# Performance work log

Measured on AMD Instinct MI355X. Metric: run time of the kernel, lower is better.

## Reference

```python
import jax, jax.numpy as jnp
import numpy as np

B, IN, E, NCLS = 1024, 784, 256, 10
BRAIN, ADIM, NJUMPS = 4, 3, 4
N = BRAIN ** ADIM  # 64 blocks
TAU = 1.0
_GKEY = jax.random.key(42)  # fixed key -> deterministic gumbel noise


def _gumbel_softmax_hard(key, logits):
    u = jax.random.uniform(key, logits.shape, minval=1e-6, maxval=1.0 - 1e-6)
    g = -jnp.log(-jnp.log(u))
    y = jax.nn.softmax((logits + g) / TAU, axis=-1)
    hard = jax.nn.one_hot(jnp.argmax(y, axis=-1), logits.shape[-1], dtype=y.dtype)
    return jax.lax.stop_gradient(hard - y) + y  # straight-through


def _next_address(state, key, at0_W1, at0_b1, at0_W2, at0_b2):
    # always uses block 0's address_transform (as in the original forward)
    h = jax.nn.relu(state @ at0_W1 + at0_b1)
    logits = (h @ at0_W2 + at0_b2).reshape(state.shape[0], ADIM, BRAIN)
    return _gumbel_softmax_hard(key, logits)  # (B, ADIM, BRAIN) one-hot


def _all_blocks(state, st_W1, st_b1, st_W2, st_b2):
    # state: (B,E); st_W*: (N,E,E) stored (in,out). Two batched GEMMs over all N blocks.
    h = jax.nn.relu(jnp.einsum('be,neh->bnh', state, st_W1) + st_b1[None])
    h = jax.nn.relu(jnp.einsum('bnh,nhg->bng', h, st_W2) + st_b2[None])
    norm = jnp.linalg.norm(state, axis=1, keepdims=True)  # (B,1), norm of INPUT state
    return h / (norm[:, :, None] + 1e-6)  # (B,N,E)


def _flatten_onehot(oh):
    # (B, ADIM, BRAIN) -> (B, BRAIN**ADIM) via iterated outer product
    b = oh.shape[0]
    fw = oh[:, 0, :]
    for d in range(1, oh.shape[1]):
        fw = (fw[:, :, None] * oh[:, d, None, :]).reshape(b, -1)
    return fw


def _forward(x, W_emb, b_emb, st_W1, st_b1, st_W2, st_b2,
             at0_W1, at0_b1, at0_W2, at0_b2, out_W1, out_b1, out_W2, out_b2):
    bsz = x.shape[0]
    state = x.reshape(bsz, -1) @ W_emb + b_emb
    initial_state = state
    current_address = _next_address(state, jax.random.fold_in(_GKEY, 0),
                                    at0_W1, at0_b1, at0_W2, at0_b2)
    exited = jnp.zeros((bsz,), dtype=bool)
    exit_states = jnp.zeros_like(state)
    exit_addresses = jnp.zeros_like(current_address)
    for i in range(NJUMPS):  # fixed small jump count; early-break replaced by masking (same math)
        active = ~exited
        bw = _flatten_onehot(current_address)                      # (B,N)
        allout = _all_blocks(state, st_W1, st_b1, st_W2, st_b2)    # (B,N,E)
        new_state = jnp.einsum('bn,bne->be', bw, allout)
        new_address = _next_address(new_state, jax.random.fold_in(_GKEY, i + 1),
                                    at0_W1, at0_b1, at0_W2, at0_b2)
        idx = jnp.argmax(new_address, axis=2)
        is_origin = jnp.all(idx == 0, axis=1) & active
        exit_states = jnp.where(is_origin[:, None], new_state, exit_states)
        exit_addresses = jnp.where(is_origin[:, None, None], new_address, exit_addresses)
        exited = exited | is_origin
        state = jnp.where(active[:, None], new_state, state)
        current_address = jnp.where(active[:, None, None], new_address, current_address)
    final_address = jnp.where(exited[:, None, None], exit_addresses, current_address)
    bw = _flatten_onehot(final_address)
    # original code computes block_out twice and keeps the one using `state` (bug-faithful)
    allout = _all_blocks(state, st_W1, st_b1, st_W2, st_b2)
    final_output = jnp.einsum('bn,bne->be', bw, allout) + initial_state
    h = jax.nn.relu(final_output @ out_W1 + out_b1)
    return h @ out_W2 + out_b2  # (B, NCLS)


def setup_inputs() -> dict:
    key = jax.random.key(0)
    ks = jax.random.split(key, 16)
    s = 0.02
    return {
        'x': jax.random.normal(ks[0], (B, IN), jnp.float32),
        'W_emb': jax.random.normal(ks[1], (IN, E), jnp.float32) * s,
        'b_emb': jnp.zeros((E,), jnp.float32),
        'st_W1': jax.random.normal(ks[2], (N, E, E), jnp.float32) * s,
        'st_b1': jnp.zeros((N, E), jnp.float32),
        'st_W2': jax.random.normal(ks[3], (N, E, E), jnp.float32) * s,
        'st_b2': jnp.zeros((N, E), jnp.float32),
        'at0_W1': jax.random.normal(ks[4], (E, E), jnp.float32) * s,
        'at0_b1': jnp.zeros((E,), jnp.float32),
        'at0_W2': jax.random.normal(ks[5], (E, ADIM * BRAIN), jnp.float32) * s,
        'at0_b2': jnp.zeros((ADIM * BRAIN,), jnp.float32),
        'out_W1': jax.random.normal(ks[6], (E, E), jnp.float32) * s,
        'out_b1': jnp.zeros((E,), jnp.float32),
        'out_W2': jax.random.normal(ks[7], (E, NCLS), jnp.float32) * s,
        'out_b2': jnp.zeros((NCLS,), jnp.float32),
    }


def reference(x, W_emb, b_emb, st_W1, st_b1, st_W2, st_b2,
              at0_W1, at0_b1, at0_W2, at0_b2, out_W1, out_b1, out_W2, out_b2):
    return _forward(x, W_emb, b_emb, st_W1, st_b1, st_W2, st_b2,
                    at0_W1, at0_b1, at0_W2, at0_b2, out_W1, out_b1, out_W2, out_b2)
```

## Files before the change

### kernel.cpp

```cpp
#include <hip/hip_runtime.h>
#include <stdint.h>


#define BATCH 1024
#define EDIM  256
#define INDIM 784
#define CH    4
#define GRID_B 304

__host__ __device__ inline uint32_t rotl32(uint32_t x, uint32_t d) {
  return (x << d) | (x >> (32u - d));
}
__host__ __device__ inline void threefry2x32(uint32_t k0, uint32_t k1,
                                             uint32_t x0, uint32_t x1,
                                             uint32_t* o0, uint32_t* o1) {
  uint32_t ks2 = k0 ^ k1 ^ 0x1BD11BDAu;
  x0 += k0; x1 += k1;
#define TF_R(a) { x0 += x1; x1 = rotl32(x1, a); x1 ^= x0; }
  TF_R(13) TF_R(15) TF_R(26) TF_R(6)   x0 += k1;  x1 += ks2 + 1u;
  TF_R(17) TF_R(29) TF_R(16) TF_R(24)  x0 += ks2; x1 += k0  + 2u;
  TF_R(13) TF_R(15) TF_R(26) TF_R(6)   x0 += k0;  x1 += k1  + 3u;
  TF_R(17) TF_R(29) TF_R(16) TF_R(24)  x0 += k1;  x1 += ks2 + 4u;
  TF_R(13) TF_R(15) TF_R(26) TF_R(6)   x0 += ks2; x1 += k0  + 5u;
#undef TF_R
  *o0 = x0; *o1 = x1;
}
__device__ inline uint32_t jax_bits12288(uint32_t k0, uint32_t k1, uint32_t L) {
  uint32_t o0, o1;
  if (L < 6144u) { threefry2x32(k0, k1, L, L + 6144u, &o0, &o1); return o0; }
  else           { threefry2x32(k0, k1, L - 6144u, L, &o0, &o1); return o1; }
}
__device__ inline float jax_uniform(uint32_t bits) {
  const float minv = 1e-6f;
  const float maxv = (float)(1.0 - 1e-06);
  const float span = maxv - minv;
  uint32_t fb = (bits >> 9) | 0x3f800000u;
  float f = __uint_as_float(fb) - 1.0f;
  float u = __fadd_rn(__fmul_rn(f, span), minv);
  return fmaxf(minv, u);
}
__device__ inline float gumbel_val(int s, int b, int c) {
  uint32_t fk0, fk1;
  threefry2x32(0u, 42u, 0u, (uint32_t)s, &fk0, &fk1);
  const uint32_t L = (uint32_t)(b * 12 + c);
  const float u = jax_uniform(jax_bits12288(fk0, fk1, L));
  return -logf(-logf(u));
}
__device__ inline int addr_argmax(const float* v) {
  int i0 = 0, i1 = 0, i2 = 0;
  { float b = v[0];
    for (int c = 1; c < 4; c++) { float x = v[c];     if (x > b) { b = x; i0 = c; } } }
  { float b = v[4];
    for (int c = 1; c < 4; c++) { float x = v[4 + c]; if (x > b) { b = x; i1 = c; } } }
  { float b = v[8];
    for (int c = 1; c < 4; c++) { float x = v[8 + c]; if (x > b) { b = x; i2 = c; } } }
  return i0 * 16 + i1 * 4 + i2;
}

#define LDW16(dst, Wc, kkq)                                                     \
  { _Pragma("unroll")                                                           \
    for (int _q = 0; _q < 4; _q++) {                                            \
      _Pragma("unroll")                                                         \
      for (int _cc = 0; _cc < 4; _cc++)                                         \
        dst[_q * 4 + _cc] = (Wc)[(size_t)((kkq) + _q) * EDIM + _cc * 64];       \
    } }

#define FMA16(acc, wv, XSarr, SROW, kabs)                                       \
  { const float4 _r0 = *(const float4*)&(XSarr)[0 * (SROW) + (kabs)];           \
    const float4 _r1 = *(const float4*)&(XSarr)[1 * (SROW) + (kabs)];           \
    const float4 _r2 = *(const float4*)&(XSarr)[2 * (SROW) + (kabs)];           \
    const float4 _r3 = *(const float4*)&(XSarr)[3 * (SROW) + (kabs)];           \
    _Pragma("unroll")                                                           \
    for (int _cc = 0; _cc < 4; _cc++) {                                         \
      acc[0][_cc] = fmaf(_r0.x, wv[0 + _cc], acc[0][_cc]);                      \
      acc[0][_cc] = fmaf(_r0.y, wv[4 + _cc], acc[0][_cc]);                      \
      acc[0][_cc] = fmaf(_r0.z, wv[8 + _cc], acc[0][_cc]);                      \
      acc[0][_cc] = fmaf(_r0.w, wv[12 + _cc], acc[0][_cc]);                     \
      acc[1][_cc] = fmaf(_r1.x, wv[0 + _cc], acc[1][_cc]);                      \
      acc[1][_cc] = fmaf(_r1.y, wv[4 + _cc], acc[1][_cc]);                      \
      acc[1][_cc] = fmaf(_r1.z, wv[8 + _cc], acc[1][_cc]);                      \
      acc[1][_cc] = fmaf(_r1.w, wv[12 + _cc], acc[1][_cc]);                     \
      acc[2][_cc] = fmaf(_r2.x, wv[0 + _cc], acc[2][_cc]);                      \
      acc[2][_cc] = fmaf(_r2.y, wv[4 + _cc], acc[2][_cc]);                      \
      acc[2][_cc] = fmaf(_r2.z, wv[8 + _cc], acc[2][_cc]);                      \
      acc[2][_cc] = fmaf(_r2.w, wv[12 + _cc], acc[2][_cc]);                     \
      acc[3][_cc] = fmaf(_r3.x, wv[0 + _cc], acc[3][_cc]);                      \
      acc[3][_cc] = fmaf(_r3.y, wv[4 + _cc], acc[3][_cc]);                      \
      acc[3][_cc] = fmaf(_r3.z, wv[8 + _cc], acc[3][_cc]);                      \
      acc[3][_cc] = fmaf(_r3.w, wv[12 + _cc], acc[3][_cc]);                     \
    } }

#define GEMM_TILE(Wbase, XSarr, SROW, kb, KS, acc)                              \
  { const float* _Wc = (Wbase) + (size_t)(kb) * EDIM + jc;                      \
    float _wvA[16], _wvB[16];                                                   \
    LDW16(_wvA, _Wc, 0)                                                         \
    _Pragma("unroll 1")                                                         \
    for (int _kk = 0; _kk < (KS); _kk += 8) {                                   \
      LDW16(_wvB, _Wc, _kk + 4)                                                 \
      FMA16(acc, _wvA, XSarr, SROW, (kb) + _kk)                                 \
      if (_kk + 8 < (KS)) LDW16(_wvA, _Wc, _kk + 8)                             \
      FMA16(acc, _wvB, XSarr, SROW, (kb) + _kk + 4)                             \
    } }

#define FMA16H(acc, wv, Harr, kabs)                                             \
  { _Pragma("unroll")                                                           \
    for (int _q = 0; _q < 4; _q++) {                                            \
      const float4 _h = *(const float4*)&(Harr)[((kabs) + _q) * 4];             \
      _Pragma("unroll")                                                         \
      for (int _cc = 0; _cc < 4; _cc++) {                                       \
        acc[0][_cc] = fmaf(_h.x, wv[_q * 4 + _cc], acc[0][_cc]);                \
        acc[1][_cc] = fmaf(_h.y, wv[_q * 4 + _cc], acc[1][_cc]);                \
        acc[2][_cc] = fmaf(_h.z, wv[_q * 4 + _cc], acc[2][_cc]);                \
        acc[3][_cc] = fmaf(_h.w, wv[_q * 4 + _cc], acc[3][_cc]);                \
      } } }

#define GEMM_TILE_H(Wbase, Harr, kb, KS, acc)                                   \
  { const float* _Wc = (Wbase) + (size_t)(kb) * EDIM + jc;                      \
    float _wvA[16], _wvB[16];                                                   \
    LDW16(_wvA, _Wc, 0)                                                         \
    _Pragma("unroll 1")                                                         \
    for (int _kk = 0; _kk < (KS); _kk += 8) {                                   \
      LDW16(_wvB, _Wc, _kk + 4)                                                 \
      FMA16H(acc, _wvA, Harr, (kb) + _kk)                                       \
      if (_kk + 8 < (KS)) LDW16(_wvA, _Wc, _kk + 8)                             \
      FMA16H(acc, _wvB, Harr, (kb) + _kk + 4)                                   \
    } }

#define P_STORE(P, kg, jc, acc)                                                 \
  { _Pragma("unroll")                                                           \
    for (int _cc = 0; _cc < 4; _cc++) {                                         \
      const int _col = (jc) + _cc * 64;                                         \
      *(float4*)&(P)[(((kg) * 256) + _col) * 4] =                               \
        make_float4(acc[0][_cc], acc[1][_cc], acc[2][_cc], acc[3][_cc]);        \
    } }

#define P_REDUCE8(P, col, bias, dst4)                                           \
  { float4 _ps = *(const float4*)&(P)[(col) * 4];                               \
    _Pragma("unroll")                                                           \
    for (int _pw = 1; _pw < 8; _pw++) {                                         \
      const float4 _pp = *(const float4*)&(P)[((_pw * 256) + (col)) * 4];       \
      _ps.x += _pp.x; _ps.y += _pp.y; _ps.z += _pp.z; _ps.w += _pp.w;           \
    }                                                                           \
    _ps.x += (bias); _ps.y += (bias); _ps.z += (bias); _ps.w += (bias);         \
    dst4 = _ps; }

#define ADDR_TAIL(P, H, P2a, vals, ab1, aW2, ab2, astep, ROWEXPR)               \
  { if (t < 256) {                                                              \
      float4 s; P_REDUCE8(P, t, (ab1)[t], s);                                   \
      *(float4*)&(H)[t * 4] = make_float4(fmaxf(s.x, 0.f), fmaxf(s.y, 0.f),     \
                                          fmaxf(s.z, 0.f), fmaxf(s.w, 0.f));    \
    }                                                                           \
    __syncthreads();                                                            \
    { const int c = t & 15, ksl = t >> 4;                                       \
      float a2[4] = {0.f, 0.f, 0.f, 0.f};                                       \
      if (c < 12) {                                                             \
        const int k0 = ksl * 8;                                                 \
        _Pragma("unroll")                                                       \
        for (int k = k0; k < k0 + 8; k++) {                                     \
          const float4 h = *(const float4*)&(H)[k * 4];                         \
          const float w = (aW2)[k * 12 + c];                                    \
          a2[0] = fmaf(h.x, w, a2[0]); a2[1] = fmaf(h.y, w, a2[1]);             \
          a2[2] = fmaf(h.z, w, a2[2]); a2[3] = fmaf(h.w, w, a2[3]);             \
        }                                                                       \
      }                                                                         \
      *(float4*)&(P2a)[(ksl * 16 + c) * 4] = make_float4(a2[0], a2[1], a2[2], a2[3]); \
    }                                                                           \
    __syncthreads();                                                            \
    if (t < 48) {                                                               \
      const int i = t / 12, c = t % 12;                                         \
      float s = 0.f;                                                            \
      _Pragma("unroll")                                                         \
      for (int w = 0; w < 32; w++) s += (P2a)[(w * 16 + c) * 4 + i];            \
      (vals)[i * 12 + c] = s + (ab2)[c] + gumbel_val((astep), (ROWEXPR), c);    \
    }                                                                           \
    __syncthreads();                                                            \
  }

__global__ __launch_bounds__(512, 2) void k_embed_a0(
    const float* __restrict__ x, const float* __restrict__ Wemb,
    const float* __restrict__ bemb,
    const float* __restrict__ aW1, const float* __restrict__ ab1,
    const float* __restrict__ aW2, const float* __restrict__ ab2,
    float* __restrict__ state, float* __restrict__ initial,
    int* __restrict__ nn_all) {
  __shared__ __align__(16) float XS[4 * INDIM];
  __shared__ __align__(16) float P[8 * 256 * 4];
  __shared__ __align__(16) float SS[4 * EDIM];
  __shared__ __align__(16) float H[EDIM * 4];
  __shared__ __align__(16) float P2a[32 * 16 * 4];
  __shared__ float vals[4 * 12];
  const int t = threadIdx.x, b0 = blockIdx.x * 4;
  const int jc = t & 63, kg = t >> 6;

  { const float4* src = (const float4*)(x + (size_t)b0 * INDIM);
    for (int p = t; p < INDIM; p += 512) ((float4*)XS)[p] = src[p];
  }
  __syncthreads();

  {
    const int kb = (kg < 2) ? kg * 104 : 208 + (kg - 2) * 96;
    float acc[4][4] = {};
    if (kg < 2) { GEMM_TILE(Wemb, XS, INDIM, kb, 104, acc); }
    else        { GEMM_TILE(Wemb, XS, INDIM, kb, 96, acc); }
    P_STORE(P, kg, jc, acc);
  }
  __syncthreads();
  if (t < 256) {
    float4 s; P_REDUCE8(P, t, bemb[t], s);
    SS[0 * EDIM + t] = s.x; SS[1 * EDIM + t] = s.y;
    SS[2 * EDIM + t] = s.z; SS[3 * EDIM + t] = s.w;
    state[(size_t)(b0 + 0) * EDIM + t] = s.x; initial[(size_t)(b0 + 0) * EDIM + t] = s.x;
    state[(size_t)(b0 + 1) * EDIM + t] = s.y; initial[(size_t)(b0 + 1) * EDIM + t] = s.y;
    state[(size_t)(b0 + 2) * EDIM + t] = s.z; initial[(size_t)(b0 + 2) * EDIM + t] = s.z;
    state[(size_t)(b0 + 3) * EDIM + t] = s.w; initial[(size_t)(b0 + 3) * EDIM + t] = s.w;
  }
  __syncthreads();

  {
    const int kb = kg * 32;
    float acc[4][4] = {};
    GEMM_TILE(aW1, SS, EDIM, kb, 32, acc);
    P_STORE(P, kg, jc, acc);
  }
  __syncthreads();
  ADDR_TAIL(P, H, P2a, vals, ab1, aW2, ab2, 0, b0 + i);
  if (t < 4) nn_all[b0 + t] = addr_argmax(&vals[t * 12]);
}

#define B_ROUTE(nnval_expr)                                                     \
  if (t < 64) hist[t] = 0;                                                      \
  if (t < 4) rowsl[t] = 0;                                                      \
  __syncthreads();                                                              \
  int myv[2]; bool fl[2];                                                       \
  _Pragma("unroll")                                                             \
  for (int p = 0; p < 2; p++) {                                                 \
    const int rr = p * 512 + t;                                                 \
    myv[p] = (nnval_expr);                                                      \
    if (myv[p] >= 0) atomicAdd(&hist[myv[p]], 1);                               \
  }                                                                             \
  __syncthreads();                                                              \
  if (t < 64) {                                                                 \
    const int cnt = hist[t];                                                    \
    const int nch = (cnt + CH - 1) / CH;                                        \
    int icnt = cnt, inch = nch;                                                 \
    _Pragma("unroll")                                                           \
    for (int d = 1; d < 64; d <<= 1) {                                          \
      int t1 = __shfl_up(icnt, d), t2 = __shfl_up(inch, d);                     \
      if (t >= d) { icnt += t1; inch += t2; }                                   \
    }                                                                           \
    const int ench = inch - nch;                                                \
    if (t == 63) meta[3] = inch;                                                \
    if (c >= ench && c < ench + nch) {                                          \
      meta[0] = t; meta[1] = c - ench;                                          \
      meta[2] = min(CH, cnt - (c - ench) * CH);                                 \
    }                                                                           \
  }                                                                             \
  __syncthreads();                                                              \
  if (c >= meta[3]) return;                                                     \
  const int n = meta[0], local = meta[1], m = meta[2];                          \
  {                                                                             \
    const int wid = t >> 6, lane = t & 63;                                      \
    unsigned long long bals[2];                                                 \
    _Pragma("unroll")                                                           \
    for (int p = 0; p < 2; p++) {                                               \
      fl[p] = (myv[p] == n);                                                    \
      bals[p] = __ballot(fl[p]);                                                \
      if (lane == 0) wcnt2[p * 8 + wid] = __popcll(bals[p]);                    \
    }                                                                           \
    __syncthreads();                                                            \
    if (t == 0) { int s = 0;                                                    \
      for (int e = 0; e < 16; e++) { wbase2[e] = s; s += wcnt2[e]; } }          \
    __syncthreads();                                                            \
    const int r0 = local * CH;                                                  \
    _Pragma("unroll")                                                           \
    for (int p = 0; p < 2; p++) {                                               \
      if (fl[p]) {                                                              \
        const int rank = wbase2[p * 8 + wid] +                                  \
          __popcll(bals[p] & ((1ull << lane) - 1ull));                          \
        if (rank >= r0 && rank < r0 + CH) rowsl[rank - r0] = p * 512 + t;       \
      }                                                                         \
    }                                                                           \
    __syncthreads();                                                            \
  }

__global__ __launch_bounds__(512, 2) void k_block_mid(
    float* __restrict__ state,
    const float* __restrict__ W1, const float* __restrict__ b1,
    const float* __restrict__ W2, const float* __restrict__ b2,
    const float* __restrict__ aW1, const float* __restrict__ ab1,
    const float* __restrict__ aW2, const float* __restrict__ ab2,
    int* __restrict__ nn_all, int rstep) {
  __shared__ __align__(16) float XS[4 * EDIM];
  __shared__ __align__(16) float P[8 * 256 * 4];
  __shared__ __align__(16) float H[EDIM * 4];
  __shared__ __align__(16) float P2a[32 * 16 * 4];
  __shared__ float vals[4 * 12];
  __shared__ int hist[64], meta[4], rowsl[4];
  __shared__ int wcnt2[16], wbase2[16];
  __shared__ float denom[4];
  const int t = threadIdx.x;
  const int c = ((blockIdx.x & 7) * 38) + (blockIdx.x >> 3);
  const int jc = t & 63, kg = t >> 6;
  const int* nnj = nn_all + rstep * BATCH;

  B_ROUTE(nnj[rr])

  if (t < 256) {
    const int i = t >> 6, q = t & 63;
    const int row = rowsl[min(i, m - 1)] & 1023;
    const float4 v = *(const float4*)(state + (size_t)row * EDIM + q * 4);
    ((float4*)XS)[t] = v;
    float sq = v.x * v.x + v.y * v.y + v.z * v.z + v.w * v.w;
#pragma unroll
    for (int d = 32; d >= 1; d >>= 1) sq += __shfl_xor(sq, d);
    if (q == 0) denom[i] = sqrtf(sq) + 1e-6f;
  }
  __syncthreads();

  const float* W1n = W1 + (size_t)n * EDIM * EDIM;
  const float* W2n = W2 + (size_t)n * EDIM * EDIM;
  const int kb = kg * 32;
  { float acc[4][4] = {};
    GEMM_TILE(W1n, XS, EDIM, kb, 32, acc);
    P_STORE(P, kg, jc, acc);
  }
  __syncthreads();
  if (t < 256) {
    float4 s; P_REDUCE8(P, t, b1[(size_t)n * EDIM + t], s);
    *(float4*)&H[t * 4] = make_float4(fmaxf(s.x, 0.f), fmaxf(s.y, 0.f),
                                      fmaxf(s.z, 0.f), fmaxf(s.w, 0.f));
  }
  __syncthreads();
  { float acc[4][4] = {};
    GEMM_TILE_H(W2n, H, kb, 32, acc);
    P_STORE(P, kg, jc, acc);
  }
  __syncthreads();
  if (t < 256) {
    float4 s; P_REDUCE8(P, t, b2[(size_t)n * EDIM + t], s);
    float sv[4] = { s.x, s.y, s.z, s.w };
#pragma unroll
    for (int i = 0; i < 4; i++) {
      if (i < m) {
        const int row = rowsl[i] & 1023;
        const float v = fmaxf(sv[i], 0.f) / denom[i];
        state[(size_t)row * EDIM + t] = v;
        XS[i * EDIM + t] = v;
      }
    }
  }
  __syncthreads();

  { float acc[4][4] = {};
    GEMM_TILE(aW1, XS, EDIM, kb, 32, acc);
    P_STORE(P, kg, jc, acc);
  }
  __syncthreads();
  ADDR_TAIL(P, H, P2a, vals, ab1, aW2, ab2, rstep + 1, (rowsl[i] & 1023));
  if (t < m) {
    const int b = rowsl[t] & 1023;
    const int nn = addr_argmax(&vals[t * 12]);
    const int s = rstep + 1;
    if (s < 4) {
      if (nn == 0) {
        for (int q = s; q <= 4; q++) nn_all[q * BATCH + b] = -1;
      } else nn_all[s * BATCH + b] = nn;
    } else nn_all[4 * BATCH + b] = nn;
  }
}

__global__ __launch_bounds__(512, 2) void k_block_final(
    const float* __restrict__ state,
    const float* __restrict__ W1, const float* __restrict__ b1,
    const float* __restrict__ W2, const float* __restrict__ b2,
    const float* __restrict__ initial,
    const float* __restrict__ oW1, const float* __restrict__ ob1,
    const float* __restrict__ oW2, const float* __restrict__ ob2,
    const int* __restrict__ nn4, float* __restrict__ out) {
  __shared__ __align__(16) float XS[4 * EDIM];
  __shared__ __align__(16) float P[8 * 256 * 4];
  __shared__ __align__(16) float H[EDIM * 4];
  __shared__ __align__(16) float P2h[32 * 16 * 4];
  __shared__ int hist[64], meta[4], rowsl[4];
  __shared__ int wcnt2[16], wbase2[16];
  __shared__ float denom[4];
  const int t = threadIdx.x;
  const int c = ((blockIdx.x & 7) * 38) + (blockIdx.x >> 3);
  const int jc = t & 63, kg = t >> 6;

  B_ROUTE(max(nn4[rr], 0))

  if (t < 256) {
    const int i = t >> 6, q = t & 63;
    const int row = rowsl[min(i, m - 1)] & 1023;
    const float4 v = *(const float4*)(state + (size_t)row * EDIM + q * 4);
    ((float4*)XS)[t] = v;
    float sq = v.x * v.x + v.y * v.y + v.z * v.z + v.w * v.w;
#pragma unroll
    for (int d = 32; d >= 1; d >>= 1) sq += __shfl_xor(sq, d);
    if (q == 0) denom[i] = sqrtf(sq) + 1e-6f;
  }
  __syncthreads();

  const float* W1n = W1 + (size_t)n * EDIM * EDIM;
  const float* W2n = W2 + (size_t)n * EDIM * EDIM;
  const int kb = kg * 32;
  { float acc[4][4] = {};
    GEMM_TILE(W1n, XS, EDIM, kb, 32, acc);
    P_STORE(P, kg, jc, acc);
  }
  __syncthreads();
  if (t < 256) {
    float4 s; P_REDUCE8(P, t, b1[(size_t)n * EDIM + t], s);
    *(float4*)&H[t * 4] = make_float4(fmaxf(s.x, 0.f), fmaxf(s.y, 0.f),
                                      fmaxf(s.z, 0.f), fmaxf(s.w, 0.f));
  }
  __syncthreads();
  { float acc[4][4] = {};
    GEMM_TILE_H(W2n, H, kb, 32, acc);
    P_STORE(P, kg, jc, acc);
  }
  __syncthreads();
  if (t < 256) {
    float4 s; P_REDUCE8(P, t, b2[(size_t)n * EDIM + t], s);
    float sv[4] = { s.x, s.y, s.z, s.w };
#pragma unroll
    for (int i = 0; i < 4; i++) {
      const int row = rowsl[i] & 1023;
      float v = fmaxf(sv[i], 0.f) / denom[i];
      v += initial[(size_t)row * EDIM + t];
      XS[i * EDIM + t] = v;
    }
  }
  __syncthreads();

  { float acc[4][4] = {};
    GEMM_TILE(oW1, XS, EDIM, kb, 32, acc);
    P_STORE(P, kg, jc, acc);
  }
  __syncthreads();
  if (t < 256) {
    float4 s; P_REDUCE8(P, t, ob1[t], s);
    *(float4*)&H[t * 4] = make_float4(fmaxf(s.x, 0.f), fmaxf(s.y, 0.f),
                                      fmaxf(s.z, 0.f), fmaxf(s.w, 0.f));
  }
  __syncthreads();
  {
    const int cc = t & 15, ksl = t >> 4;
    float a2[4] = {0.f, 0.f, 0.f, 0.f};
    if (cc < 10) {
      const int k0 = ksl * 8;
#pragma unroll
      for (int k = k0; k < k0 + 8; k++) {
        const float4 h = *(const float4*)&H[k * 4];
        const float w = oW2[k * 10 + cc];
        a2[0] = fmaf(h.x, w, a2[0]); a2[1] = fmaf(h.y, w, a2[1]);
        a2[2] = fmaf(h.z, w, a2[2]); a2[3] = fmaf(h.w, w, a2[3]);
      }
    }
    *(float4*)&P2h[(ksl * 16 + cc) * 4] = make_float4(a2[0], a2[1], a2[2], a2[3]);
  }
  __syncthreads();
  if (t < 40) {
    const int i = t / 10, cc = t % 10;
    if (i < m) {
      float s = 0.f;
#pragma unroll
      for (int w = 0; w < 32; w++) s += P2h[(w * 16 + cc) * 4 + i];
      const int row = rowsl[i] & 1023;
      out[(size_t)row * 10 + cc] = s + ob2[cc];
    }
  }
}

extern "C" void kernel_launch(void* const* d_in, const int* in_sizes, int n_in,
                              void* d_out, int out_size, void* d_ws, size_t ws_size,
                              hipStream_t stream) {
  const float* x    = (const float*)d_in[0];
  const float* Wemb = (const float*)d_in[1];
  const float* bemb = (const float*)d_in[2];
  const float* stW1 = (const float*)d_in[3];
  const float* stb1 = (const float*)d_in[4];
  const float* stW2 = (const float*)d_in[5];
  const float* stb2 = (const float*)d_in[6];
  const float* aW1  = (const float*)d_in[7];
  const float* ab1  = (const float*)d_in[8];
  const float* aW2  = (const float*)d_in[9];
  const float* ab2  = (const float*)d_in[10];
  const float* oW1  = (const float*)d_in[11];
  const float* ob1  = (const float*)d_in[12];
  const float* oW2  = (const float*)d_in[13];
  const float* ob2  = (const float*)d_in[14];
  float* out = (float*)d_out;

  char* ws = (char*)d_ws;
  auto alloc = [&](size_t bytes) { char* p = ws; ws += (bytes + 255) & ~(size_t)255; return p; };
  float* state   = (float*)alloc((size_t)BATCH * EDIM * 4);
  float* initial = (float*)alloc((size_t)BATCH * EDIM * 4);
  int*   nn_all  = (int*)alloc(5 * BATCH * 4);

  k_embed_a0<<<BATCH / 4, 512, 0, stream>>>(x, Wemb, bemb, aW1, ab1, aW2, ab2,
                                            state, initial, nn_all);
  for (int j = 0; j < 4; j++)
    k_block_mid<<<GRID_B, 512, 0, stream>>>(state, stW1, stb1, stW2, stb2,
                                            aW1, ab1, aW2, ab2, nn_all, j);
  k_block_final<<<GRID_B, 512, 0, stream>>>(state, stW1, stb1, stW2, stb2,
                                            initial, oW1, ob1, oW2, ob2,
                                            nn_all + 4 * BATCH, out);
}
```

Measured before the change: 231.3 us.

## Process eight rows per block in routed block GEMMs and split embed/address kernels

Doubles the number of batch rows handled per workgroup in the routed block-MLP kernels (CH 4→8, fewer blocks), reshaping each thread's tile to 8 rows × 2 columns with 4 k-partitions instead of 8. Each weight element loaded from global memory is reused across more rows, so per-expert weight traffic falls. The fused embed+address kernel is also split into a column-split embed kernel and a separate address kernel. The cost is fewer workgroups (less parallelism, with more rounding waste when an expert gets a partial group of rows), more register pressure, and one extra kernel launch.

New measurement: 243.1 us. 1.05x slower.

```diff
diff --git a/kernel.cpp b/kernel.cpp
--- a/kernel.cpp
+++ b/kernel.cpp
@@ -5,8 +5,8 @@
 #define BATCH 1024
 #define EDIM  256
 #define INDIM 784
-#define CH    4
-#define GRID_B 304
+#define CH    8
+#define GRID_B 192
 
 __host__ __device__ inline uint32_t rotl32(uint32_t x, uint32_t d) {
   return (x << d) | (x >> (32u - d));
@@ -57,179 +57,207 @@
   return i0 * 16 + i1 * 4 + i2;
 }
 
-#define LDW16(dst, Wc, kkq)                                                     \
+#define LDW8(dst, Wc, kkq, CSTR)                                                \
   { _Pragma("unroll")                                                           \
     for (int _q = 0; _q < 4; _q++) {                                            \
       _Pragma("unroll")                                                         \
-      for (int _cc = 0; _cc < 4; _cc++)                                         \
-        dst[_q * 4 + _cc] = (Wc)[(size_t)((kkq) + _q) * EDIM + _cc * 64];       \
+      for (int _cc = 0; _cc < 2; _cc++)                                         \
+        dst[_q * 2 + _cc] = (Wc)[(size_t)((kkq) + _q) * EDIM + _cc * (CSTR)];   \
     } }
 
-#define FMA16(acc, wv, XSarr, SROW, kabs)                                       \
+#define FMA_ROW(acc, ri, rv, wv)                                                \
+  acc[ri][0] = fmaf(rv.x, wv[0], acc[ri][0]);                                   \
+  acc[ri][0] = fmaf(rv.y, wv[2], acc[ri][0]);                                   \
+  acc[ri][0] = fmaf(rv.z, wv[4], acc[ri][0]);                                   \
+  acc[ri][0] = fmaf(rv.w, wv[6], acc[ri][0]);                                   \
+  acc[ri][1] = fmaf(rv.x, wv[1], acc[ri][1]);                                   \
+  acc[ri][1] = fmaf(rv.y, wv[3], acc[ri][1]);                                   \
+  acc[ri][1] = fmaf(rv.z, wv[5], acc[ri][1]);                                   \
+  acc[ri][1] = fmaf(rv.w, wv[7], acc[ri][1]);
+
+#define FMA32(acc, wv, XSarr, SROW, kabs)                                       \
   { const float4 _r0 = *(const float4*)&(XSarr)[0 * (SROW) + (kabs)];           \
     const float4 _r1 = *(const float4*)&(XSarr)[1 * (SROW) + (kabs)];           \
     const float4 _r2 = *(const float4*)&(XSarr)[2 * (SROW) + (kabs)];           \
     const float4 _r3 = *(const float4*)&(XSarr)[3 * (SROW) + (kabs)];           \
-    _Pragma("unroll")                                                           \
-    for (int _cc = 0; _cc < 4; _cc++) {                                         \
-      acc[0][_cc] = fmaf(_r0.x, wv[0 + _cc], acc[0][_cc]);                      \
-      acc[0][_cc] = fmaf(_r0.y, wv[4 + _cc], acc[0][_cc]);                      \
-      acc[0][_cc] = fmaf(_r0.z, wv[8 + _cc], acc[0][_cc]);                      \
-      acc[0][_cc] = fmaf(_r0.w, wv[12 + _cc], acc[0][_cc]);                     \
-      acc[1][_cc] = fmaf(_r1.x, wv[0 + _cc], acc[1][_cc]);                      \
-      acc[1][_cc] = fmaf(_r1.y, wv[4 + _cc], acc[1][_cc]);                      \
-      acc[1][_cc] = fmaf(_r1.z, wv[8 + _cc], acc[1][_cc]);                      \
-      acc[1][_cc] = fmaf(_r1.w, wv[12 + _cc], acc[1][_cc]);                     \
-      acc[2][_cc] = fmaf(_r2.x, wv[0 + _cc], acc[2][_cc]);                      \
-      acc[2][_cc] = fmaf(_r2.y, wv[4 + _cc], acc[2][_cc]);                      \
-      acc[2][_cc] = fmaf(_r2.z, wv[8 + _cc], acc[2][_cc]);                      \
-      acc[2][_cc] = fmaf(_r2.w, wv[12 + _cc], acc[2][_cc]);                     \
-      acc[3][_cc] = fmaf(_r3.x, wv[0 + _cc], acc[3][_cc]);                      \
-      acc[3][_cc] = fmaf(_r3.y, wv[4 + _cc], acc[3][_cc]);                      \
-      acc[3][_cc] = fmaf(_r3.z, wv[8 + _cc], acc[3][_cc]);                      \
-      acc[3][_cc] = fmaf(_r3.w, wv[12 + _cc], acc[3][_cc]);                     \
-    } }
-
-#define GEMM_TILE(Wbase, XSarr, SROW, kb, KS, acc)                              \
-  { const float* _Wc = (Wbase) + (size_t)(kb) * EDIM + jc;                      \
-    float _wvA[16], _wvB[16];                                                   \
-    LDW16(_wvA, _Wc, 0)                                                         \
+    const float4 _r4 = *(const float4*)&(XSarr)[4 * (SROW) + (kabs)];           \
+    const float4 _r5 = *(const float4*)&(XSarr)[5 * (SROW) + (kabs)];           \
+    const float4 _r6 = *(const float4*)&(XSarr)[6 * (SROW) + (kabs)];           \
+    const float4 _r7 = *(const float4*)&(XSarr)[7 * (SROW) + (kabs)];           \
+    FMA_ROW(acc, 0, _r0, wv) FMA_ROW(acc, 1, _r1, wv)                           \
+    FMA_ROW(acc, 2, _r2, wv) FMA_ROW(acc, 3, _r3, wv)                           \
+    FMA_ROW(acc, 4, _r4, wv) FMA_ROW(acc, 5, _r5, wv)                           \
+    FMA_ROW(acc, 6, _r6, wv) FMA_ROW(acc, 7, _r7, wv) }
+
+#define GEMM_TILE8(Wbase, COLB, CSTR, XSarr, SROW, kb, KS, acc)                 \
+  { const float* _Wc = (Wbase) + (size_t)(kb) * EDIM + (COLB);                  \
+    float _wvA[8], _wvB[8];                                                     \
+    LDW8(_wvA, _Wc, 0, CSTR)                                                    \
     _Pragma("unroll 1")                                                         \
     for (int _kk = 0; _kk < (KS); _kk += 8) {                                   \
-      LDW16(_wvB, _Wc, _kk + 4)                                                 \
-      FMA16(acc, _wvA, XSarr, SROW, (kb) + _kk)                                 \
-      if (_kk + 8 < (KS)) LDW16(_wvA, _Wc, _kk + 8)                             \
-      FMA16(acc, _wvB, XSarr, SROW, (kb) + _kk + 4)                             \
+      LDW8(_wvB, _Wc, _kk + 4, CSTR)                                            \
+      FMA32(acc, _wvA, XSarr, SROW, (kb) + _kk)                                 \
+      if (_kk + 8 < (KS)) LDW8(_wvA, _Wc, _kk + 8, CSTR)                        \
+      FMA32(acc, _wvB, XSarr, SROW, (kb) + _kk + 4)                             \
     } }
 
-#define FMA16H(acc, wv, Harr, kabs)                                             \
+#define FMA32H(acc, wv, Harr, kabs)                                             \
   { _Pragma("unroll")                                                           \
     for (int _q = 0; _q < 4; _q++) {                                            \
-      const float4 _h = *(const float4*)&(Harr)[((kabs) + _q) * 4];             \
+      const float4 _hl = *(const float4*)&(Harr)[((kabs) + _q) * 8];            \
+      const float4 _hh = *(const float4*)&(Harr)[((kabs) + _q) * 8 + 4];        \
       _Pragma("unroll")                                                         \
-      for (int _cc = 0; _cc < 4; _cc++) {                                       \
-        acc[0][_cc] = fmaf(_h.x, wv[_q * 4 + _cc], acc[0][_cc]);                \
-        acc[1][_cc] = fmaf(_h.y, wv[_q * 4 + _cc], acc[1][_cc]);                \
-        acc[2][_cc] = fmaf(_h.z, wv[_q * 4 + _cc], acc[2][_cc]);                \
-        acc[3][_cc] = fmaf(_h.w, wv[_q * 4 + _cc], acc[3][_cc]);                \
+      for (int _cc = 0; _cc < 2; _cc++) {                                       \
+        acc[0][_cc] = fmaf(_hl.x, wv[_q * 2 + _cc], acc[0][_cc]);               \
+        acc[1][_cc] = fmaf(_hl.y, wv[_q * 2 + _cc], acc[1][_cc]);               \
+        acc[2][_cc] = fmaf(_hl.z, wv[_q * 2 + _cc], acc[2][_cc]);               \
+        acc[3][_cc] = fmaf(_hl.w, wv[_q * 2 + _cc], acc[3][_cc]);               \
+        acc[4][_cc] = fmaf(_hh.x, wv[_q * 2 + _cc], acc[4][_cc]);               \
+        acc[5][_cc] = fmaf(_hh.y, wv[_q * 2 + _cc], acc[5][_cc]);               \
+        acc[6][_cc] = fmaf(_hh.z, wv[_q * 2 + _cc], acc[6][_cc]);               \
+        acc[7][_cc] = fmaf(_hh.w, wv[_q * 2 + _cc], acc[7][_cc]);               \
       } } }
 
-#define GEMM_TILE_H(Wbase, Harr, kb, KS, acc)                                   \
-  { const float* _Wc = (Wbase) + (size_t)(kb) * EDIM + jc;                      \
-    float _wvA[16], _wvB[16];                                                   \
-    LDW16(_wvA, _Wc, 0)                                                         \
+#define GEMM_TILE_H8(Wbase, COLB, CSTR, Harr, kb, KS, acc)                      \
+  { const float* _Wc = (Wbase) + (size_t)(kb) * EDIM + (COLB);                  \
+    float _wvA[8], _wvB[8];                                                     \
+    LDW8(_wvA, _Wc, 0, CSTR)                                                    \
     _Pragma("unroll 1")                                                         \
     for (int _kk = 0; _kk < (KS); _kk += 8) {                                   \
-      LDW16(_wvB, _Wc, _kk + 4)                                                 \
-      FMA16H(acc, _wvA, Harr, (kb) + _kk)                                       \
-      if (_kk + 8 < (KS)) LDW16(_wvA, _Wc, _kk + 8)                             \
-      FMA16H(acc, _wvB, Harr, (kb) + _kk + 4)                                   \
+      LDW8(_wvB, _Wc, _kk + 4, CSTR)                                            \
+      FMA32H(acc, _wvA, Harr, (kb) + _kk)                                       \
+      if (_kk + 8 < (KS)) LDW8(_wvA, _Wc, _kk + 8, CSTR)                        \
+      FMA32H(acc, _wvB, Harr, (kb) + _kk + 4)                                   \
     } }
 
-#define P_STORE(P, kg, jc, acc)                                                 \
+#define P_STORE8(P, kg, NCOL, LCOL, CSTR, acc)                                  \
   { _Pragma("unroll")                                                           \
-    for (int _cc = 0; _cc < 4; _cc++) {                                         \
-      const int _col = (jc) + _cc * 64;                                         \
-      *(float4*)&(P)[(((kg) * 256) + _col) * 4] =                               \
+    for (int _cc = 0; _cc < 2; _cc++) {                                         \
+      const int _col = (LCOL) + _cc * (CSTR);                                   \
+      *(float4*)&(P)[(((kg) * (NCOL)) + _col) * 8] =                            \
         make_float4(acc[0][_cc], acc[1][_cc], acc[2][_cc], acc[3][_cc]);        \
+      *(float4*)&(P)[(((kg) * (NCOL)) + _col) * 8 + 4] =                        \
+        make_float4(acc[4][_cc], acc[5][_cc], acc[6][_cc], acc[7][_cc]);        \
     } }
 
-#define P_REDUCE8(P, col, bias, dst4)                                           \
-  { float4 _ps = *(const float4*)&(P)[(col) * 4];                               \
+#define P_REDUCE(P, col, NCOL, NPART, bias, lo4, hi4)                           \
+  { lo4 = *(const float4*)&(P)[(col) * 8];                                      \
+    hi4 = *(const float4*)&(P)[(col) * 8 + 4];                                  \
     _Pragma("unroll")                                                           \
-    for (int _pw = 1; _pw < 8; _pw++) {                                         \
-      const float4 _pp = *(const float4*)&(P)[((_pw * 256) + (col)) * 4];       \
-      _ps.x += _pp.x; _ps.y += _pp.y; _ps.z += _pp.z; _ps.w += _pp.w;           \
-    }                                                                           \
-    _ps.x += (bias); _ps.y += (bias); _ps.z += (bias); _ps.w += (bias);         \
-    dst4 = _ps; }
-
-#define ADDR_TAIL(P, H, P2a, vals, ab1, aW2, ab2, astep, ROWEXPR)               \
+    for (int _pw = 1; _pw < (NPART); _pw++) {                                   \
+      const float4 _pl = *(const float4*)&(P)[((_pw * (NCOL)) + (col)) * 8];    \
+      const float4 _ph = *(const float4*)&(P)[((_pw * (NCOL)) + (col)) * 8 + 4];\
+      lo4.x += _pl.x; lo4.y += _pl.y; lo4.z += _pl.z; lo4.w += _pl.w;           \
+      hi4.x += _ph.x; hi4.y += _ph.y; hi4.z += _ph.z; hi4.w += _ph.w;           \
+    }                                                                           \
+    lo4.x += (bias); lo4.y += (bias); lo4.z += (bias); lo4.w += (bias);         \
+    hi4.x += (bias); hi4.y += (bias); hi4.z += (bias); hi4.w += (bias); }
+
+#define ADDR_TAIL8(P, H, P2a, vals, ab1, aW2, ab2, astep, ROWEXPR)              \
   { if (t < 256) {                                                              \
-      float4 s; P_REDUCE8(P, t, (ab1)[t], s);                                   \
-      *(float4*)&(H)[t * 4] = make_float4(fmaxf(s.x, 0.f), fmaxf(s.y, 0.f),     \
-                                          fmaxf(s.z, 0.f), fmaxf(s.w, 0.f));    \
+      float4 lo, hi; P_REDUCE(P, t, 256, 4, (ab1)[t], lo, hi);                  \
+      *(float4*)&(H)[t * 8] = make_float4(fmaxf(lo.x, 0.f), fmaxf(lo.y, 0.f),   \
+                                          fmaxf(lo.z, 0.f), fmaxf(lo.w, 0.f));  \
+      *(float4*)&(H)[t * 8 + 4] = make_float4(fmaxf(hi.x, 0.f), fmaxf(hi.y, 0.f),\
+                                              fmaxf(hi.z, 0.f), fmaxf(hi.w, 0.f));\
     }                                                                           \
     __syncthreads();                                                            \
     { const int c = t & 15, ksl = t >> 4;                                       \
-      float a2[4] = {0.f, 0.f, 0.f, 0.f};                                       \
+      float a2[8] = {0.f,0.f,0.f,0.f,0.f,0.f,0.f,0.f};                          \
       if (c < 12) {                                                             \
         const int k0 = ksl * 8;                                                 \
         _Pragma("unroll")                                                       \
         for (int k = k0; k < k0 + 8; k++) {                                     \
-          const float4 h = *(const float4*)&(H)[k * 4];                         \
+          const float4 hl = *(const float4*)&(H)[k * 8];                        \
+          const float4 hh = *(const float4*)&(H)[k * 8 + 4];                    \
           const float w = (aW2)[k * 12 + c];                                    \
-          a2[0] = fmaf(h.x, w, a2[0]); a2[1] = fmaf(h.y, w, a2[1]);             \
-          a2[2] = fmaf(h.z, w, a2[2]); a2[3] = fmaf(h.w, w, a2[3]);             \
+          a2[0] = fmaf(hl.x, w, a2[0]); a2[1] = fmaf(hl.y, w, a2[1]);           \
+          a2[2] = fmaf(hl.z, w, a2[2]); a2[3] = fmaf(hl.w, w, a2[3]);           \
+          a2[4] = fmaf(hh.x, w, a2[4]); a2[5] = fmaf(hh.y, w, a2[5]);           \
+          a2[6] = fmaf(hh.z, w, a2[6]); a2[7] = fmaf(hh.w, w, a2[7]);           \
         }                                                                       \
       }                                                                         \
-      *(float4*)&(P2a)[(ksl * 16 + c) * 4] = make_float4(a2[0], a2[1], a2[2], a2[3]); \
+      *(float4*)&(P2a)[(ksl * 16 + c) * 8] = make_float4(a2[0], a2[1], a2[2], a2[3]); \
+      *(float4*)&(P2a)[(ksl * 16 + c) * 8 + 4] = make_float4(a2[4], a2[5], a2[6], a2[7]); \
     }                                                                           \
     __syncthreads();                                                            \
-    if (t < 48) {                                                               \
+    if (t < 96) {                                                               \
       const int i = t / 12, c = t % 12;                                         \
       float s = 0.f;                                                            \
       _Pragma("unroll")                                                         \
-      for (int w = 0; w < 32; w++) s += (P2a)[(w * 16 + c) * 4 + i];            \
+      for (int w = 0; w < 32; w++) s += (P2a)[(w * 16 + c) * 8 + i];            \
       (vals)[i * 12 + c] = s + (ab2)[c] + gumbel_val((astep), (ROWEXPR), c);    \
     }                                                                           \
     __syncthreads();                                                            \
   }
 
-__global__ __launch_bounds__(512, 2) void k_embed_a0(
+__global__ __launch_bounds__(512, 2) void k_embed(
     const float* __restrict__ x, const float* __restrict__ Wemb,
     const float* __restrict__ bemb,
+    float* __restrict__ state, float* __restrict__ initial) {
+  __shared__ __align__(16) float XS[8 * INDIM];
+  __shared__ __align__(16) float P[8 * 128 * 8];
+  const int t = threadIdx.x;
+  const int rg = blockIdx.x >> 1, chh = blockIdx.x & 1;
+  const int b0 = rg * 8;
+  const int jch = t & 63, kg8 = t >> 6;
+
+  { const float4* src = (const float4*)(x + (size_t)b0 * INDIM);
+    for (int p = t; p < (8 * INDIM) / 4; p += 512) ((float4*)XS)[p] = src[p];
+  }
+  __syncthreads();
+
+  {
+    const int kb = (kg8 < 2) ? kg8 * 104 : 208 + (kg8 - 2) * 96;
+    const int KS = (kg8 < 2) ? 104 : 96;
+    float acc[8][2] = {};
+    if (kg8 < 2) { GEMM_TILE8(Wemb, chh * 128 + jch, 64, XS, INDIM, kb, 104, acc); }
+    else         { GEMM_TILE8(Wemb, chh * 128 + jch, 64, XS, INDIM, kb, 96, acc); }
+    (void)KS;
+    P_STORE8(P, kg8, 128, jch, 64, acc);
+  }
+  __syncthreads();
+  if (t < 128) {
+    float4 lo, hi; P_REDUCE(P, t, 128, 8, bemb[chh * 128 + t], lo, hi);
+    const int gcol = chh * 128 + t;
+    float sv[8] = { lo.x, lo.y, lo.z, lo.w, hi.x, hi.y, hi.z, hi.w };
+#pragma unroll
+    for (int i = 0; i < 8; i++) {
+      state[(size_t)(b0 + i) * EDIM + gcol] = sv[i];
+      initial[(size_t)(b0 + i) * EDIM + gcol] = sv[i];
+    }
+  }
+}
+
+__global__ __launch_bounds__(512, 2) void k_addr0(
+    const float* __restrict__ state,
     const float* __restrict__ aW1, const float* __restrict__ ab1,
     const float* __restrict__ aW2, const float* __restrict__ ab2,
-    float* __restrict__ state, float* __restrict__ initial,
     int* __restrict__ nn_all) {
-  __shared__ __align__(16) float XS[4 * INDIM];
-  __shared__ __align__(16) float P[8 * 256 * 4];
-  __shared__ __align__(16) float SS[4 * EDIM];
-  __shared__ __align__(16) float H[EDIM * 4];
-  __shared__ __align__(16) float P2a[32 * 16 * 4];
-  __shared__ float vals[4 * 12];
-  const int t = threadIdx.x, b0 = blockIdx.x * 4;
-  const int jc = t & 63, kg = t >> 6;
-
-  { const float4* src = (const float4*)(x + (size_t)b0 * INDIM);
-    for (int p = t; p < INDIM; p += 512) ((float4*)XS)[p] = src[p];
-  }
-  __syncthreads();
-
-  {
-    const int kb = (kg < 2) ? kg * 104 : 208 + (kg - 2) * 96;
-    float acc[4][4] = {};
-    if (kg < 2) { GEMM_TILE(Wemb, XS, INDIM, kb, 104, acc); }
-    else        { GEMM_TILE(Wemb, XS, INDIM, kb, 96, acc); }
-    P_STORE(P, kg, jc, acc);
-  }
-  __syncthreads();
-  if (t < 256) {
-    float4 s; P_REDUCE8(P, t, bemb[t], s);
-    SS[0 * EDIM + t] = s.x; SS[1 * EDIM + t] = s.y;
-    SS[2 * EDIM + t] = s.z; SS[3 * EDIM + t] = s.w;
-    state[(size_t)(b0 + 0) * EDIM + t] = s.x; initial[(size_t)(b0 + 0) * EDIM + t] = s.x;
-    state[(size_t)(b0 + 1) * EDIM + t] = s.y; initial[(size_t)(b0 + 1) * EDIM + t] = s.y;
-    state[(size_t)(b0 + 2) * EDIM + t] = s.z; initial[(size_t)(b0 + 2) * EDIM + t] = s.z;
-    state[(size_t)(b0 + 3) * EDIM + t] = s.w; initial[(size_t)(b0 + 3) * EDIM + t] = s.w;
-  }
-  __syncthreads();
-
-  {
-    const int kb = kg * 32;
-    float acc[4][4] = {};
-    GEMM_TILE(aW1, SS, EDIM, kb, 32, acc);
-    P_STORE(P, kg, jc, acc);
-  }
-  __syncthreads();
-  ADDR_TAIL(P, H, P2a, vals, ab1, aW2, ab2, 0, b0 + i);
-  if (t < 4) nn_all[b0 + t] = addr_argmax(&vals[t * 12]);
+  __shared__ __align__(16) float XS[8 * EDIM];
+  __shared__ __align__(16) float P[4 * 256 * 8];
+  __shared__ __align__(16) float H[EDIM * 8];
+  __shared__ float vals[8 * 12];
+  float* const P2a = P;
+  const int t = threadIdx.x, b0 = blockIdx.x * 8;
+  const int jc = t & 127, kg = t >> 7;
+
+  ((float4*)XS)[t] = ((const float4*)(state + (size_t)b0 * EDIM))[t];
+  __syncthreads();
+
+  { const int kb = kg * 64;
+    float acc[8][2] = {};
+    GEMM_TILE8(aW1, jc, 128, XS, EDIM, kb, 64, acc);
+    P_STORE8(P, kg, 256, jc, 128, acc);
+  }
+  __syncthreads();
+  ADDR_TAIL8(P, H, P2a, vals, ab1, aW2, ab2, 0, b0 + i);
+  if (t < 8) nn_all[b0 + t] = addr_argmax(&vals[t * 12]);
 }
 
 #define B_ROUTE(nnval_expr)                                                     \
   if (t < 64) hist[t] = 0;                                                      \
-  if (t < 4) rowsl[t] = 0;                                                      \
+  if (t < 8) rowsl[t] = 0;                                                      \
   __syncthreads();                                                              \
   int myv[2]; bool fl[2];                                                       \
   _Pragma("unroll")                                                             \
@@ -290,22 +318,22 @@
     const float* __restrict__ aW1, const float* __restrict__ ab1,
     const float* __restrict__ aW2, const float* __restrict__ ab2,
     int* __restrict__ nn_all, int rstep) {
-  __shared__ __align__(16) float XS[4 * EDIM];
-  __shared__ __align__(16) float P[8 * 256 * 4];
-  __shared__ __align__(16) float H[EDIM * 4];
-  __shared__ __align__(16) float P2a[32 * 16 * 4];
-  __shared__ float vals[4 * 12];
-  __shared__ int hist[64], meta[4], rowsl[4];
+  __shared__ __align__(16) float XS[8 * EDIM];
+  __shared__ __align__(16) float P[4 * 256 * 8];
+  __shared__ __align__(16) float H[EDIM * 8];
+  __shared__ float vals[8 * 12];
+  __shared__ int hist[64], meta[4], rowsl[8];
   __shared__ int wcnt2[16], wbase2[16];
-  __shared__ float denom[4];
+  __shared__ float denom[8];
+  float* const P2a = P;
   const int t = threadIdx.x;
-  const int c = ((blockIdx.x & 7) * 38) + (blockIdx.x >> 3);
-  const int jc = t & 63, kg = t >> 6;
+  const int c = ((blockIdx.x & 7) * 24) + (blockIdx.x >> 3);
+  const int jc = t & 127, kg = t >> 7;
   const int* nnj = nn_all + rstep * BATCH;
 
   B_ROUTE(nnj[rr])
 
-  if (t < 256) {
+  {
     const int i = t >> 6, q = t & 63;
     const int row = rowsl[min(i, m - 1)] & 1023;
     const float4 v = *(const float4*)(state + (size_t)row * EDIM + q * 4);
@@ -319,28 +347,30 @@
 
   const float* W1n = W1 + (size_t)n * EDIM * EDIM;
   const float* W2n = W2 + (size_t)n * EDIM * EDIM;
-  const int kb = kg * 32;
-  { float acc[4][4] = {};
-    GEMM_TILE(W1n, XS, EDIM, kb, 32, acc);
-    P_STORE(P, kg, jc, acc);
+  const int kb = kg * 64;
+  { float acc[8][2] = {};
+    GEMM_TILE8(W1n, jc, 128, XS, EDIM, kb, 64, acc);
+    P_STORE8(P, kg, 256, jc, 128, acc);
   }
   __syncthreads();
   if (t < 256) {
-    float4 s; P_REDUCE8(P, t, b1[(size_t)n * EDIM + t], s);
-    *(float4*)&H[t * 4] = make_float4(fmaxf(s.x, 0.f), fmaxf(s.y, 0.f),
-                                      fmaxf(s.z, 0.f), fmaxf(s.w, 0.f));
-  }
-  __syncthreads();
-  { float acc[4][4] = {};
-    GEMM_TILE_H(W2n, H, kb, 32, acc);
-    P_STORE(P, kg, jc, acc);
+    float4 lo, hi; P_REDUCE(P, t, 256, 4, b1[(size_t)n * EDIM + t], lo, hi);
+    *(float4*)&H[t * 8] = make_float4(fmaxf(lo.x, 0.f), fmaxf(lo.y, 0.f),
+                                      fmaxf(lo.z, 0.f), fmaxf(lo.w, 0.f));
+    *(float4*)&H[t * 8 + 4] = make_float4(fmaxf(hi.x, 0.f), fmaxf(hi.y, 0.f),
+                                          fmaxf(hi.z, 0.f), fmaxf(hi.w, 0.f));
+  }
+  __syncthreads();
+  { float acc[8][2] = {};
+    GEMM_TILE_H8(W2n, jc, 128, H, kb, 64, acc);
+    P_STORE8(P, kg, 256, jc, 128, acc);
   }
   __syncthreads();
   if (t < 256) {
-    float4 s; P_REDUCE8(P, t, b2[(size_t)n * EDIM + t], s);
-    float sv[4] = { s.x, s.y, s.z, s.w };
-#pragma unroll
-    for (int i = 0; i < 4; i++) {
+    float4 lo, hi; P_REDUCE(P, t, 256, 4, b2[(size_t)n * EDIM + t], lo, hi);
+    float sv[8] = { lo.x, lo.y, lo.z, lo.w, hi.x, hi.y, hi.z, hi.w };
+#pragma unroll
+    for (int i = 0; i < 8; i++) {
       if (i < m) {
         const int row = rowsl[i] & 1023;
         const float v = fmaxf(sv[i], 0.f) / denom[i];
@@ -351,12 +381,12 @@
   }
   __syncthreads();
 
-  { float acc[4][4] = {};
-    GEMM_TILE(aW1, XS, EDIM, kb, 32, acc);
-    P_STORE(P, kg, jc, acc);
-  }
-  __syncthreads();
-  ADDR_TAIL(P, H, P2a, vals, ab1, aW2, ab2, rstep + 1, (rowsl[i] & 1023));
+  { float acc[8][2] = {};
+    GEMM_TILE8(aW1, jc, 128, XS, EDIM, kb, 64, acc);
+    P_STORE8(P, kg, 256, jc, 128, acc);
+  }
+  __syncthreads();
+  ADDR_TAIL8(P, H, P2a, vals, ab1, aW2, ab2, rstep + 1, (rowsl[i] & 1023));
   if (t < m) {
     const int b = rowsl[t] & 1023;
     const int nn = addr_argmax(&vals[t * 12]);
@@ -377,21 +407,20 @@
     const float* __restrict__ oW1, const float* __restrict__ ob1,
     const float* __restrict__ oW2, const float* __restrict__ ob2,
     const int* __restrict__ nn4, float* __restrict__ out) {
-  __shared__ __align__(16) float XS[4 * EDIM];
-  __shared__ __align__(16) float P[8 * 256 * 4];
-  __shared__ __align__(16) float H[EDIM * 4];
-  __shared__ __align__(16) float P2h[32 * 16 * 4];
-  __shared__ int hist[64], meta[4], rowsl[4];
+  __shared__ __align__(16) float XS[8 * EDIM];
+  __shared__ __align__(16) float P[4 * 256 * 8];
+  __shared__ __align__(16) float H[EDIM * 8];
+  __shared__ int hist[64], meta[4], rowsl[8];
   __shared__ int wcnt2[16], wbase2[16];
-  __shared__ float denom[4];
+  __shared__ float denom[8];
+  float* const P2h = P;
   const int t = threadIdx.x;
-  const int c = ((blockIdx.x & 7) * 38) + (blockIdx.x >> 3);
-  const int jc = t & 63, kg = t >> 6;
+  const int c = ((blockIdx.x & 7) * 24) + (blockIdx.x >> 3);
+  const int jc = t & 127, kg = t >> 7;
 
   B_ROUTE(max(nn4[rr], 0))
 
-  if (t < 256) {
-    const int i = t >> 6, q = t & 63;
+  { const int i = t >> 6, q = t & 63;
     const int row = rowsl[min(i, m - 1)] & 1023;
     const float4 v = *(const float4*)(state + (size_t)row * EDIM + q * 4);
     ((float4*)XS)[t] = v;
@@ -404,28 +433,30 @@
 
   const float* W1n = W1 + (size_t)n * EDIM * EDIM;
   const float* W2n = W2 + (size_t)n * EDIM * EDIM;
-  const int kb = kg * 32;
-  { float acc[4][4] = {};
-    GEMM_TILE(W1n, XS, EDIM, kb, 32, acc);
-    P_STORE(P, kg, jc, acc);
+  const int kb = kg * 64;
+  { float acc[8][2] = {};
+    GEMM_TILE8(W1n, jc, 128, XS, EDIM, kb, 64, acc);
+    P_STORE8(P, kg, 256, jc, 128, acc);
   }
   __syncthreads();
   if (t < 256) {
-    float4 s; P_REDUCE8(P, t, b1[(size_t)n * EDIM + t], s);
-    *(float4*)&H[t * 4] = make_float4(fmaxf(s.x, 0.f), fmaxf(s.y, 0.f),
-                                      fmaxf(s.z, 0.f), fmaxf(s.w, 0.f));
-  }
-  __syncthreads();
-  { float acc[4][4] = {};
-    GEMM_TILE_H(W2n, H, kb, 32, acc);
-    P_STORE(P, kg, jc, acc);
+    float4 lo, hi; P_REDUCE(P, t, 256, 4, b1[(size_t)n * EDIM + t], lo, hi);
+    *(float4*)&H[t * 8] = make_float4(fmaxf(lo.x, 0.f), fmaxf(lo.y, 0.f),
+                                      fmaxf(lo.z, 0.f), fmaxf(lo.w, 0.f));
+    *(float4*)&H[t * 8 + 4] = make_float4(fmaxf(hi.x, 0.f), fmaxf(hi.y, 0.f),
+                                          fmaxf(hi.z, 0.f), fmaxf(hi.w, 0.f));
+  }
+  __syncthreads();
+  { float acc[8][2] = {};
+    GEMM_TILE_H8(W2n, jc, 128, H, kb, 64, acc);
+    P_STORE8(P, kg, 256, jc, 128, acc);
   }
   __syncthreads();
   if (t < 256) {
-    float4 s; P_REDUCE8(P, t, b2[(size_t)n * EDIM + t], s);
-    float sv[4] = { s.x, s.y, s.z, s.w };
-#pragma unroll
-    for (int i = 0; i < 4; i++) {
+    float4 lo, hi; P_REDUCE(P, t, 256, 4, b2[(size_t)n * EDIM + t], lo, hi);
+    float sv[8] = { lo.x, lo.y, lo.z, lo.w, hi.x, hi.y, hi.z, hi.w };
+#pragma unroll
+    for (int i = 0; i < 8; i++) {
       const int row = rowsl[i] & 1023;
       float v = fmaxf(sv[i], 0.f) / denom[i];
       v += initial[(size_t)row * EDIM + t];
@@ -434,39 +465,45 @@
   }
   __syncthreads();
 
-  { float acc[4][4] = {};
-    GEMM_TILE(oW1, XS, EDIM, kb, 32, acc);
-    P_STORE(P, kg, jc, acc);
+  { float acc[8][2] = {};
+    GEMM_TILE8(oW1, jc, 128, XS, EDIM, kb, 64, acc);
+    P_STORE8(P, kg, 256, jc, 128, acc);
   }
   __syncthreads();
   if (t < 256) {
-    float4 s; P_REDUCE8(P, t, ob1[t], s);
-    *(float4*)&H[t * 4] = make_float4(fmaxf(s.x, 0.f), fmaxf(s.y, 0.f),
-                                      fmaxf(s.z, 0.f), fmaxf(s.w, 0.f));
+    float4 lo, hi; P_REDUCE(P, t, 256, 4, ob1[t], lo, hi);
+    *(float4*)&H[t * 8] = make_float4(fmaxf(lo.x, 0.f), fmaxf(lo.y, 0.f),
+                                      fmaxf(lo.z, 0.f), fmaxf(lo.w, 0.f));
+    *(float4*)&H[t * 8 + 4] = make_float4(fmaxf(hi.x, 0.f), fmaxf(hi.y, 0.f),
+                                          fmaxf(hi.z, 0.f), fmaxf(hi.w, 0.f));
   }
   __syncthreads();
   {
     const int cc = t & 15, ksl = t >> 4;
-    float a2[4] = {0.f, 0.f, 0.f, 0.f};
+    float a2[8] = {0.f,0.f,0.f,0.f,0.f,0.f,0.f,0.f};
     if (cc < 10) {
       const int k0 = ksl * 8;
 #pragma unroll
       for (int k = k0; k < k0 + 8; k++) {
-        const float4 h = *(const float4*)&H[k * 4];
+        const float4 hl = *(const float4*)&H[k * 8];
+        const float4 hh = *(const float4*)&H[k * 8 + 4];
         const float w = oW2[k * 10 + cc];
-        a2[0] = fmaf(h.x, w, a2[0]); a2[1] = fmaf(h.y, w, a2[1]);
-        a2[2] = fmaf(h.z, w, a2[2]); a2[3] = fmaf(h.w, w, a2[3]);
+        a2[0] = fmaf(hl.x, w, a2[0]); a2[1] = fmaf(hl.y, w, a2[1]);
+        a2[2] = fmaf(hl.z, w, a2[2]); a2[3] = fmaf(hl.w, w, a2[3]);
+        a2[4] = fmaf(hh.x, w, a2[4]); a2[5] = fmaf(hh.y, w, a2[5]);
+        a2[6] = fmaf(hh.z, w, a2[6]); a2[7] = fmaf(hh.w, w, a2[7]);
       }
     }
-    *(float4*)&P2h[(ksl * 16 + cc) * 4] = make_float4(a2[0], a2[1], a2[2], a2[3]);
-  }
-  __syncthreads();
-  if (t < 40) {
+    *(float4*)&P2h[(ksl * 16 + cc) * 8] = make_float4(a2[0], a2[1], a2[2], a2[3]);
+    *(float4*)&P2h[(ksl * 16 + cc) * 8 + 4] = make_float4(a2[4], a2[5], a2[6], a2[7]);
+  }
+  __syncthreads();
+  if (t < 80) {
     const int i = t / 10, cc = t % 10;
     if (i < m) {
       float s = 0.f;
 #pragma unroll
-      for (int w = 0; w < 32; w++) s += P2h[(w * 16 + cc) * 4 + i];
+      for (int w = 0; w < 32; w++) s += P2h[(w * 16 + cc) * 8 + i];
       const int row = rowsl[i] & 1023;
       out[(size_t)row * 10 + cc] = s + ob2[cc];
     }
@@ -499,8 +536,8 @@
   float* initial = (float*)alloc((size_t)BATCH * EDIM * 4);
   int*   nn_all  = (int*)alloc(5 * BATCH * 4);
 
-  k_embed_a0<<<BATCH / 4, 512, 0, stream>>>(x, Wemb, bemb, aW1, ab1, aW2, ab2,
-                                            state, initial, nn_all);
+  k_embed<<<256, 512, 0, stream>>>(x, Wemb, bemb, state, initial);
+  k_addr0<<<128, 512, 0, stream>>>(state, aW1, ab1, aW2, ab2, nn_all);
   for (int j = 0; j < 4; j++)
     k_block_mid<<<GRID_B, 512, 0, stream>>>(state, stW1, stb1, stW2, stb2,
                                             aW1, ab1, aW2, ab2, nn_all, j);
```
